# Kernel tuning notes

Hardware: AMD Instinct MI355X
Metric: run time of the kernel (lower is better)

The kernel has to match this reference:

```python
import jax, jax.numpy as jnp
import numpy as np

GAMMA_MIN = -15.0
GAMMA_MAX = 10.0
REDUCE_DIMS = (-3, -2, -1)


def setup_inputs() -> dict:
    key = jax.random.key(0)
    k1, k2, k3 = jax.random.split(key, 3)
    in_tensor = jax.random.normal(k1, (8, 3, 32, 32), dtype=jnp.float32)
    normalized_gamma = jax.random.uniform(k2, (1,), dtype=jnp.float32)
    mask = jnp.ones((3, 32, 32), dtype=jnp.float32)
    training_data = jax.random.normal(k3, (2048, 3, 32, 32), dtype=jnp.float32)
    return {"in_tensor": in_tensor, "normalized_gamma": normalized_gamma,
            "mask": mask, "training_data": training_data}


def reference(in_tensor, normalized_gamma, mask, training_data):
    # scalar gamma from the first element of normalized_gamma
    gamma = normalized_gamma[0] * (GAMMA_MAX - GAMMA_MIN) + GAMMA_MIN
    variance = jax.nn.sigmoid(-gamma)
    alpha = jnp.sqrt(1.0 - variance)
    sigma = jnp.sqrt(variance)
    var_tilde = jnp.exp(-gamma)  # 1 / exp(gamma)
    state = in_tensor * jnp.sqrt(1.0 + var_tilde)  # [B,C,H,W]

    # optimal denoiser: masked L2 distance to every training sample
    # error: [B,N,C,H,W]
    error = (state[:, None, ...] - training_data[None, ...]) * mask
    sse = jnp.sum(error * error, axis=REDUCE_DIMS, keepdims=True)  # [B,N,1,1,1]
    log_likeli = -sse / (2.0 * var_tilde)
    prob = jax.nn.softmax(log_likeli, axis=1)  # softmax over training-set axis
    denoised = jnp.sum(prob * training_data[None, ...], axis=1)  # [B,C,H,W]

    eps = (in_tensor - alpha * denoised) / sigma
    return eps * mask
```

## Files before the change

### kernel.cpp

```cpp
#include <hip/hip_runtime.h>
#include <math.h>

#define B 8
#define N 2048
#define D 3072
#define K1_BLOCKS 512
#define NPB (N / K1_BLOCKS)
#define NCHUNK 128
#define CHUNK (N / NCHUNK)


struct Scalars {
    float state_scale;
    float inv_2vt;
    float alpha;
    float inv_sigma;
};

__device__ inline Scalars compute_scalars(const float* __restrict__ ng) {
    float gamma = ng[0] * 25.0f - 15.0f;
    float var_tilde = expf(-gamma);
    float variance = 1.0f / (1.0f + expf(gamma));
    Scalars s;
    s.state_scale = sqrtf(1.0f + var_tilde);
    s.inv_2vt     = 0.5f / var_tilde;
    s.alpha       = sqrtf(1.0f - variance);
    s.inv_sigma   = 1.0f / sqrtf(variance);
    return s;
}


__global__ __launch_bounds__(256, 2) void k_sse(
        const float* __restrict__ in, const float* __restrict__ ng,
        const float* __restrict__ mask, const float* __restrict__ train,
        float* __restrict__ sse_out) {
    const int tid = threadIdx.x;
    const int n0  = blockIdx.x * NPB;
    const Scalars sc = compute_scalars(ng);

    float4 sm[3][B];
    float4 m4[3];
#pragma unroll
    for (int k = 0; k < 3; ++k) {
        const int d = (tid + k * 256) * 4;
        m4[k] = *(const float4*)(mask + d);
#pragma unroll
        for (int b = 0; b < B; ++b) {
            const float4 s = *(const float4*)(in + b * D + d);
            sm[k][b].x = s.x * sc.state_scale * m4[k].x;
            sm[k][b].y = s.y * sc.state_scale * m4[k].y;
            sm[k][b].z = s.z * sc.state_scale * m4[k].z;
            sm[k][b].w = s.w * sc.state_scale * m4[k].w;
        }
    }

    __shared__ double red[NPB][4][B];
    const int wave = tid >> 6, lane = tid & 63;

#pragma unroll
    for (int j = 0; j < NPB; ++j) {
        const float* trow = train + (size_t)(n0 + j) * D;
        double acc[B];
#pragma unroll
        for (int b = 0; b < B; ++b) acc[b] = 0.0;

#pragma unroll
        for (int k = 0; k < 3; ++k) {
            const int d = (tid + k * 256) * 4;
            const float4 t = *(const float4*)(trow + d);
            float4 tm;
            tm.x = t.x * m4[k].x;
            tm.y = t.y * m4[k].y;
            tm.z = t.z * m4[k].z;
            tm.w = t.w * m4[k].w;
#pragma unroll
            for (int b = 0; b < B; ++b) {
                float dx = sm[k][b].x - tm.x;
                float dy = sm[k][b].y - tm.y;
                float dz = sm[k][b].z - tm.z;
                float dw = sm[k][b].w - tm.w;
                acc[b] += (double)dx * dx + (double)dy * dy
                        + (double)dz * dz + (double)dw * dw;
            }
        }

#pragma unroll
        for (int b = 0; b < B; ++b)
            for (int off = 32; off; off >>= 1)
                acc[b] += __shfl_down(acc[b], off);
        if (lane == 0) {
#pragma unroll
            for (int b = 0; b < B; ++b) red[j][wave][b] = acc[b];
        }
    }
    __syncthreads();
    if (tid < NPB * B) {
        const int j = tid >> 3, b = tid & 7;
        double s = red[j][0][b] + red[j][1][b] + red[j][2][b] + red[j][3][b];
        sse_out[b * N + (n0 + j)] = (float)s;
    }
}


__global__ __launch_bounds__(256) void k_softmax(
        const float* __restrict__ sse, const float* __restrict__ ng,
        float* __restrict__ probT) {
    const int b   = blockIdx.x;
    const int tid = threadIdx.x;
    const Scalars sc = compute_scalars(ng);
    const float* row = sse + b * N;

    float v[N / 256];
#pragma unroll
    for (int k = 0; k < N / 256; ++k)
        v[k] = -row[tid + k * 256] * sc.inv_2vt;

    float mx = v[0];
#pragma unroll
    for (int k = 1; k < N / 256; ++k) mx = fmaxf(mx, v[k]);
    for (int off = 32; off; off >>= 1)
        mx = fmaxf(mx, __shfl_xor(mx, off));
    __shared__ float smx[4];
    if ((tid & 63) == 0) smx[tid >> 6] = mx;
    __syncthreads();
    mx = fmaxf(fmaxf(smx[0], smx[1]), fmaxf(smx[2], smx[3]));

    float e[N / 256];
    float sum = 0.0f;
#pragma unroll
    for (int k = 0; k < N / 256; ++k) {
        e[k] = expf(v[k] - mx);
        sum += e[k];
    }
    for (int off = 32; off; off >>= 1)
        sum += __shfl_xor(sum, off);
    __shared__ float ssum[4];
    if ((tid & 63) == 0) ssum[tid >> 6] = sum;
    __syncthreads();
    const float inv = 1.0f / (ssum[0] + ssum[1] + ssum[2] + ssum[3]);

#pragma unroll
    for (int k = 0; k < N / 256; ++k)
        probT[(tid + k * 256) * B + b] = e[k] * inv;
}


__device__ inline void fma4(float4& a, float p, const float4& t) {
    a.x = fmaf(p, t.x, a.x);
    a.y = fmaf(p, t.y, a.y);
    a.z = fmaf(p, t.z, a.z);
    a.w = fmaf(p, t.w, a.w);
}

__global__ __launch_bounds__(64) void k_denoise_partial(
        const float* __restrict__ train, const float* __restrict__ probT,
        float* __restrict__ partials) {
    const int d = (blockIdx.x * 64 + threadIdx.x) * 4;
    const int c = blockIdx.y;

    float4 acc[B];
#pragma unroll
    for (int b = 0; b < B; ++b) acc[b] = make_float4(0.f, 0.f, 0.f, 0.f);

    const int n0 = c * CHUNK;
#pragma unroll
    for (int i = 0; i < CHUNK; ++i) {
        const int n = n0 + i;
        const float4 t  = *(const float4*)(train + (size_t)n * D + d);
        const float4 p0 = *(const float4*)(probT + n * B);
        const float4 p1 = *(const float4*)(probT + n * B + 4);
        fma4(acc[0], p0.x, t); fma4(acc[1], p0.y, t);
        fma4(acc[2], p0.z, t); fma4(acc[3], p0.w, t);
        fma4(acc[4], p1.x, t); fma4(acc[5], p1.y, t);
        fma4(acc[6], p1.z, t); fma4(acc[7], p1.w, t);
    }
#pragma unroll
    for (int b = 0; b < B; ++b)
        *(float4*)(partials + ((size_t)(c * B + b)) * D + d) = acc[b];
}


__global__ __launch_bounds__(64) void k_eps(
        const float* __restrict__ in, const float* __restrict__ ng,
        const float* __restrict__ mask, const float* __restrict__ partials,
        float* __restrict__ out) {
    const int i = blockIdx.x * 64 + threadIdx.x;
    const int b = i / D;
    const int d = i - b * D;
    const Scalars sc = compute_scalars(ng);

    float s = 0.0f;
#pragma unroll 16
    for (int c = 0; c < NCHUNK; ++c)
        s += partials[((size_t)(c * B + b)) * D + d];

    out[i] = (in[i] - sc.alpha * s) * sc.inv_sigma * mask[d];
}


extern "C" void kernel_launch(void* const* d_in, const int* in_sizes, int n_in,
                              void* d_out, int out_size, void* d_ws, size_t ws_size,
                              hipStream_t stream) {
    const float* in    = (const float*)d_in[0];
    const float* ng    = (const float*)d_in[1];
    const float* mask  = (const float*)d_in[2];
    const float* train = (const float*)d_in[3];
    float* out = (float*)d_out;

    float* ws       = (float*)d_ws;
    float* sse      = ws;
    float* probT    = ws + B * N;
    float* partials = ws + 2 * B * N;

    k_sse<<<K1_BLOCKS, 256, 0, stream>>>(in, ng, mask, train, sse);
    k_softmax<<<B, 256, 0, stream>>>(sse, ng, probT);
    k_denoise_partial<<<dim3(D / 4 / 64, NCHUNK), 64, 0, stream>>>(train, probT, partials);
    k_eps<<<(B * D) / 64, 64, 0, stream>>>(in, ng, mask, partials, out);
}
```

Measured before the change: 37.99 us.

## Fuse SSE, softmax and weighted sum per chunk with online-softmax combine

Replaces the four-kernel pipeline with a per-chunk kernel. Each chunk computes distances, a local max-shifted exponent and the weighted training sum, and a combine kernel merges the chunks with a rescaled log-sum-exp. This removes the global softmax pass, the probability buffer and two launches, and reads each training row within one block. In exchange, grid parallelism for the distance phase drops to 128 blocks, and the per-thread partial sums are reduced in float rather than double.

```diff
diff --git a/kernel.cpp b/kernel.cpp
--- a/kernel.cpp
+++ b/kernel.cpp
@@ -4,10 +4,9 @@
 #define B 8
 #define N 2048
 #define D 3072
-#define K1_BLOCKS 512
-#define NPB (N / K1_BLOCKS)
 #define NCHUNK 128
 #define CHUNK (N / NCHUNK)
+#define K2_BPB (D / 256)
 
 
 struct Scalars {
@@ -29,13 +28,22 @@
     return s;
 }
 
-
-__global__ __launch_bounds__(256, 2) void k_sse(
+__device__ inline void fma4(float4& a, float p, const float4& t) {
+    a.x = fmaf(p, t.x, a.x);
+    a.y = fmaf(p, t.y, a.y);
+    a.z = fmaf(p, t.z, a.z);
+    a.w = fmaf(p, t.w, a.w);
+}
+
+
+__global__ __launch_bounds__(256) void k_chunk(
         const float* __restrict__ in, const float* __restrict__ ng,
         const float* __restrict__ mask, const float* __restrict__ train,
-        float* __restrict__ sse_out) {
+        float* __restrict__ partials, float* __restrict__ cmin,
+        float* __restrict__ cden) {
     const int tid = threadIdx.x;
-    const int n0  = blockIdx.x * NPB;
+    const int c   = blockIdx.x;
+    const int n0  = c * CHUNK;
     const Scalars sc = compute_scalars(ng);
 
     float4 sm[3][B];
@@ -54,11 +62,14 @@
         }
     }
 
-    __shared__ double red[NPB][4][B];
+    __shared__ float red[CHUNK][4][B];
+    __shared__ float sse_s[CHUNK][B];
+    __shared__ float u_s[CHUNK][B];
+    __shared__ float smin[B];
     const int wave = tid >> 6, lane = tid & 63;
 
-#pragma unroll
-    for (int j = 0; j < NPB; ++j) {
+#pragma unroll 1
+    for (int j = 0; j < CHUNK; ++j) {
         const float* trow = train + (size_t)(n0 + j) * D;
         double acc[B];
 #pragma unroll
@@ -79,122 +90,93 @@
                 float dy = sm[k][b].y - tm.y;
                 float dz = sm[k][b].z - tm.z;
                 float dw = sm[k][b].w - tm.w;
-                acc[b] += (double)dx * dx + (double)dy * dy
-                        + (double)dz * dz + (double)dw * dw;
+                float s4 = fmaf(dx, dx, fmaf(dy, dy, fmaf(dz, dz, dw * dw)));
+                acc[b] += (double)s4;
             }
         }
-
+#pragma unroll
+        for (int b = 0; b < B; ++b) {
+            float f = (float)acc[b];
+            for (int off = 32; off; off >>= 1)
+                f += __shfl_down(f, off);
+            if (lane == 0) red[j][wave][b] = f;
+        }
+    }
+    __syncthreads();
+    if (tid < CHUNK * B) {
+        const int j = tid >> 3, b = tid & 7;
+        sse_s[j][b] = red[j][0][b] + red[j][1][b] + red[j][2][b] + red[j][3][b];
+    }
+    __syncthreads();
+
+    if (tid < B) {
+        float m = sse_s[0][tid];
+#pragma unroll
+        for (int j = 1; j < CHUNK; ++j) m = fminf(m, sse_s[j][tid]);
+        smin[tid] = m;
+    }
+    __syncthreads();
+    if (tid < CHUNK * B) {
+        const int j = tid >> 3, b = tid & 7;
+        u_s[j][b] = expf((smin[b] - sse_s[j][b]) * sc.inv_2vt);
+    }
+    __syncthreads();
+    if (tid < B) {
+        float s = 0.0f;
+#pragma unroll
+        for (int j = 0; j < CHUNK; ++j) s += u_s[j][tid];
+        cden[c * B + tid] = s;
+        cmin[c * B + tid] = smin[tid];
+    }
+
+#pragma unroll
+    for (int k = 0; k < 3; ++k) {
+        const int d = (tid + k * 256) * 4;
+        float4 acc[B];
+#pragma unroll
+        for (int b = 0; b < B; ++b) acc[b] = make_float4(0.f, 0.f, 0.f, 0.f);
+#pragma unroll
+        for (int j = 0; j < CHUNK; ++j) {
+            const float4 t  = *(const float4*)(train + (size_t)(n0 + j) * D + d);
+            const float4 u0 = *(const float4*)&u_s[j][0];
+            const float4 u1 = *(const float4*)&u_s[j][4];
+            fma4(acc[0], u0.x, t); fma4(acc[1], u0.y, t);
+            fma4(acc[2], u0.z, t); fma4(acc[3], u0.w, t);
+            fma4(acc[4], u1.x, t); fma4(acc[5], u1.y, t);
+            fma4(acc[6], u1.z, t); fma4(acc[7], u1.w, t);
+        }
 #pragma unroll
         for (int b = 0; b < B; ++b)
-            for (int off = 32; off; off >>= 1)
-                acc[b] += __shfl_down(acc[b], off);
-        if (lane == 0) {
-#pragma unroll
-            for (int b = 0; b < B; ++b) red[j][wave][b] = acc[b];
-        }
-    }
-    __syncthreads();
-    if (tid < NPB * B) {
-        const int j = tid >> 3, b = tid & 7;
-        double s = red[j][0][b] + red[j][1][b] + red[j][2][b] + red[j][3][b];
-        sse_out[b * N + (n0 + j)] = (float)s;
-    }
-}
-
-
-__global__ __launch_bounds__(256) void k_softmax(
-        const float* __restrict__ sse, const float* __restrict__ ng,
-        float* __restrict__ probT) {
-    const int b   = blockIdx.x;
-    const int tid = threadIdx.x;
-    const Scalars sc = compute_scalars(ng);
-    const float* row = sse + b * N;
-
-    float v[N / 256];
-#pragma unroll
-    for (int k = 0; k < N / 256; ++k)
-        v[k] = -row[tid + k * 256] * sc.inv_2vt;
-
-    float mx = v[0];
-#pragma unroll
-    for (int k = 1; k < N / 256; ++k) mx = fmaxf(mx, v[k]);
-    for (int off = 32; off; off >>= 1)
-        mx = fmaxf(mx, __shfl_xor(mx, off));
-    __shared__ float smx[4];
-    if ((tid & 63) == 0) smx[tid >> 6] = mx;
-    __syncthreads();
-    mx = fmaxf(fmaxf(smx[0], smx[1]), fmaxf(smx[2], smx[3]));
-
-    float e[N / 256];
-    float sum = 0.0f;
-#pragma unroll
-    for (int k = 0; k < N / 256; ++k) {
-        e[k] = expf(v[k] - mx);
-        sum += e[k];
-    }
-    for (int off = 32; off; off >>= 1)
-        sum += __shfl_xor(sum, off);
-    __shared__ float ssum[4];
-    if ((tid & 63) == 0) ssum[tid >> 6] = sum;
-    __syncthreads();
-    const float inv = 1.0f / (ssum[0] + ssum[1] + ssum[2] + ssum[3]);
-
-#pragma unroll
-    for (int k = 0; k < N / 256; ++k)
-        probT[(tid + k * 256) * B + b] = e[k] * inv;
-}
-
-
-__device__ inline void fma4(float4& a, float p, const float4& t) {
-    a.x = fmaf(p, t.x, a.x);
-    a.y = fmaf(p, t.y, a.y);
-    a.z = fmaf(p, t.z, a.z);
-    a.w = fmaf(p, t.w, a.w);
-}
-
-__global__ __launch_bounds__(64) void k_denoise_partial(
-        const float* __restrict__ train, const float* __restrict__ probT,
-        float* __restrict__ partials) {
-    const int d = (blockIdx.x * 64 + threadIdx.x) * 4;
-    const int c = blockIdx.y;
-
-    float4 acc[B];
-#pragma unroll
-    for (int b = 0; b < B; ++b) acc[b] = make_float4(0.f, 0.f, 0.f, 0.f);
-
-    const int n0 = c * CHUNK;
-#pragma unroll
-    for (int i = 0; i < CHUNK; ++i) {
-        const int n = n0 + i;
-        const float4 t  = *(const float4*)(train + (size_t)n * D + d);
-        const float4 p0 = *(const float4*)(probT + n * B);
-        const float4 p1 = *(const float4*)(probT + n * B + 4);
-        fma4(acc[0], p0.x, t); fma4(acc[1], p0.y, t);
-        fma4(acc[2], p0.z, t); fma4(acc[3], p0.w, t);
-        fma4(acc[4], p1.x, t); fma4(acc[5], p1.y, t);
-        fma4(acc[6], p1.z, t); fma4(acc[7], p1.w, t);
-    }
-#pragma unroll
-    for (int b = 0; b < B; ++b)
-        *(float4*)(partials + ((size_t)(c * B + b)) * D + d) = acc[b];
-}
-
-
-__global__ __launch_bounds__(64) void k_eps(
+            *(float4*)(partials + ((size_t)(c * B + b)) * D + d) = acc[b];
+    }
+}
+
+
+__global__ __launch_bounds__(256) void k_combine(
         const float* __restrict__ in, const float* __restrict__ ng,
         const float* __restrict__ mask, const float* __restrict__ partials,
+        const float* __restrict__ cmin, const float* __restrict__ cden,
         float* __restrict__ out) {
-    const int i = blockIdx.x * 64 + threadIdx.x;
-    const int b = i / D;
-    const int d = i - b * D;
+    const int tid = threadIdx.x;
+    const int b   = blockIdx.x / K2_BPB;
+    const int d   = (blockIdx.x % K2_BPB) * 256 + tid;
     const Scalars sc = compute_scalars(ng);
 
-    float s = 0.0f;
+    float M = -INFINITY;
 #pragma unroll 16
     for (int c = 0; c < NCHUNK; ++c)
-        s += partials[((size_t)(c * B + b)) * D + d];
-
-    out[i] = (in[i] - sc.alpha * s) * sc.inv_sigma * mask[d];
+        M = fmaxf(M, -cmin[c * B + b] * sc.inv_2vt);
+
+    float s = 0.0f, den = 0.0f;
+#pragma unroll 16
+    for (int c = 0; c < NCHUNK; ++c) {
+        const float w = expf(-cmin[c * B + b] * sc.inv_2vt - M);
+        den = fmaf(w, cden[c * B + b], den);
+        s   = fmaf(w, partials[((size_t)(c * B + b)) * D + d], s);
+    }
+
+    const int i = b * D + d;
+    out[i] = (in[i] - sc.alpha * (s / den)) * sc.inv_sigma * mask[d];
 }
 
 
@@ -208,12 +190,12 @@
     float* out = (float*)d_out;
 
     float* ws       = (float*)d_ws;
-    float* sse      = ws;
-    float* probT    = ws + B * N;
-    float* partials = ws + 2 * B * N;
-
-    k_sse<<<K1_BLOCKS, 256, 0, stream>>>(in, ng, mask, train, sse);
-    k_softmax<<<B, 256, 0, stream>>>(sse, ng, probT);
-    k_denoise_partial<<<dim3(D / 4 / 64, NCHUNK), 64, 0, stream>>>(train, probT, partials);
-    k_eps<<<(B * D) / 64, 64, 0, stream>>>(in, ng, mask, partials, out);
-}
+    float* partials = ws;
+    float* cmin     = ws + (size_t)NCHUNK * B * D;
+    float* cden     = cmin + NCHUNK * B;
+
+    k_chunk<<<NCHUNK, 256, 0, stream>>>(in, ng, mask, train,
+                                        partials, cmin, cden);
+    k_combine<<<B * K2_BPB, 256, 0, stream>>>(in, ng, mask, partials,
+                                              cmin, cden, out);
+}
```

After: 88.67 us. 2.33x slower.
